# Kernel tuning notes

Measured on AMD Instinct MI355X. Metric: run time of the kernel, lower is better.

Reference implementation:

```python
import jax, jax.numpy as jnp
import numpy as np

T, B, IN_DIM = 8192, 4, 512
D_V, D_K, CHUNK = 512, 64, 128
EPS = 1e-8


def setup_inputs() -> dict:
    key = jax.random.key(0)
    ks = jax.random.split(key, 9)
    s = 0.02
    return {
        "x": jax.random.normal(ks[0], (T, B, IN_DIM), jnp.float32),
        "Wv": jax.random.normal(ks[1], (D_V, IN_DIM), jnp.float32) * s,
        "bv": jnp.zeros((D_V,), jnp.float32),
        "Wk": jax.random.normal(ks[2], (D_K, IN_DIM), jnp.float32) * s,
        "bk": jnp.zeros((D_K,), jnp.float32),
        "Wq": jax.random.normal(ks[3], (D_K, IN_DIM), jnp.float32) * s,
        "bq": jnp.zeros((D_K,), jnp.float32),
        "Wa": jax.random.normal(ks[4], (D_K, IN_DIM), jnp.float32) * s,
        "ba": jnp.zeros((D_K,), jnp.float32),
    }


def reference(x, Wv, bv, Wk, bk, Wq, bq, Wa, ba):
    # Projections: x (T, B, in_dim)
    v = x @ Wv.T + bv                      # (T, B, d)
    k = x @ Wk.T + bk                      # (T, B, n)
    q = x @ Wq.T + bq                      # (T, B, n)
    alpha = jax.nn.sigmoid(x @ Wa.T + ba)  # (T, B, n) decay gates

    Tt, Bb = x.shape[0], x.shape[1]
    C = CHUNK
    nC = Tt // C  # T assumed divisible by chunk size

    def to_chunks(a):
        return a.reshape(nC, C, Bb, a.shape[-1])

    vs, ks_, qs, als = to_chunks(v), to_chunks(k), to_chunks(q), to_chunks(alpha)
    causal = jnp.tril(jnp.ones((C, C), dtype=bool))  # (C, C)

    def body(S, inp):
        v_ch, k_ch, q_ch, a_ch = inp  # each (C, B, .)
        # Cumulative decay product within chunk (clamped as in the original)
        p = jnp.cumprod(jnp.maximum(a_ch, EPS), axis=0)      # (C, B, n)
        q_t = q_ch * p                                        # (C, B, n)
        k_t = k_ch / (p + EPS)                                # (C, B, n)
        # Intra-chunk causal attention scores
        A = jnp.einsum('tbn,sbn->bts', q_t, k_t)              # (B, C, C)
        A = jnp.where(causal[None, :, :], A, jnp.zeros((), A.dtype))
        y = jnp.einsum('bts,sbd->tbd', A, v_ch)               # intra-chunk
        y = y + jnp.einsum('bdn,tbn->tbd', S, q_t)            # cross-chunk carry
        # State update to end of chunk
        p_end = p[-1]                                         # (B, n)
        S_writes = jnp.einsum('tbd,tbn->bdn', v_ch, k_t * p_end[None, :, :])
        S_new = S * p_end[:, None, :] + S_writes              # (B, d, n)
        return S_new, y

    S0 = jnp.zeros((Bb, D_V, D_K), x.dtype)
    _, ys = jax.lax.scan(body, S0, (vs, ks_, qs, als))        # ys: (nC, C, B, d)
    return ys.reshape(Tt, Bb, D_V)
```

## Files before the change

### kernel.cpp

```cpp
#include <hip/hip_runtime.h>
#include <math.h>

#define T_DIM 8192
#define B_DIM 4
#define INDIM 512
#define DV 512
#define DK 64
#define CHUNK 128
#define NCH (T_DIM / CHUNK)
#define ROWS (T_DIM * B_DIM)
#define NPAD 768
#define KCAT 192
#define EPSF 1e-8f

typedef float float4_t __attribute__((ext_vector_type(4)));
typedef short short8_t __attribute__((ext_vector_type(8)));
typedef _Float16 half8_t __attribute__((ext_vector_type(8)));

__device__ inline unsigned short f2bf(float f) {
  unsigned int u = __float_as_uint(f);
  unsigned int r = (u + 0x7fffu + ((u >> 16) & 1u)) >> 16;
  return (unsigned short)r;
}
__device__ inline float bf2f(unsigned short h) {
  return __uint_as_float(((unsigned int)h) << 16);
}
__device__ inline unsigned short f2h(float f) {
  _Float16 h = (_Float16)f;
  unsigned short u;
  __builtin_memcpy(&u, &h, 2);
  return u;
}

__device__ inline void gload16(const void* g, void* l) {
  __builtin_amdgcn_global_load_lds(
      (const __attribute__((address_space(1))) void*)g,
      (__attribute__((address_space(3))) void*)l, 16, 0, 0);
}

__global__ __launch_bounds__(256) void cast_kernel(
    const float* __restrict__ x,
    const float* __restrict__ Wv, const float* __restrict__ Wk,
    const float* __restrict__ Wq, const float* __restrict__ Wa,
    const float* __restrict__ bv, const float* __restrict__ bk,
    const float* __restrict__ bq, const float* __restrict__ ba,
    unsigned short* __restrict__ xh, unsigned short* __restrict__ wh,
    float* __restrict__ bcat)
{
  if (blockIdx.x < 16384) {
    const size_t i4 = ((size_t)blockIdx.x * 256 + threadIdx.x) * 4;
    const float4 v = *(const float4*)&x[i4];
    ushort4 h;
    h.x = f2h(v.x); h.y = f2h(v.y); h.z = f2h(v.z); h.w = f2h(v.w);
    *(ushort4*)&xh[i4] = h;
  } else {
    const int t = (blockIdx.x - 16384) * 256 + threadIdx.x;
    const size_t i4 = (size_t)t * 4;
    const int row = (int)(i4 >> 9);
    const int col = (int)(i4 & 511);
    float4 v = {0.f, 0.f, 0.f, 0.f};
    if (row < 512)      v = *(const float4*)&Wv[(size_t)row * INDIM + col];
    else if (row < 576) v = *(const float4*)&Wk[(size_t)(row - 512) * INDIM + col];
    else if (row < 640) v = *(const float4*)&Wq[(size_t)(row - 576) * INDIM + col];
    else if (row < 704) v = *(const float4*)&Wa[(size_t)(row - 640) * INDIM + col];
    ushort4 h;
    h.x = f2h(v.x); h.y = f2h(v.y); h.z = f2h(v.z); h.w = f2h(v.w);
    *(ushort4*)&wh[i4] = h;
    if (t < NPAD) {
      float b = 0.f;
      if (t < 512)      b = bv[t];
      else if (t < 576) b = bk[t - 512];
      else if (t < 640) b = bq[t - 576];
      else if (t < 704) b = ba[t - 640];
      bcat[t] = b;
    }
  }
}

__global__ __launch_bounds__(256) void proj_mfma_kernel(
    const unsigned short* __restrict__ xh, const unsigned short* __restrict__ wh,
    const float* __restrict__ bcat,
    unsigned short* __restrict__ Bt_h, unsigned short* __restrict__ Bt_l,
    float* __restrict__ k_ws, float* __restrict__ q_ws,
    float* __restrict__ a_ws)
{
  __shared__ __align__(16) _Float16 Ah[3][128 * 32];
  __shared__ __align__(16) _Float16 Bh[3][128 * 32];

  const int d     = blockIdx.x;
  const int grp   = d >> 3;
  const int ytile = (d & 7) * 32 + grp / 6;
  const int xtile = grp % 6;
  const int r0 = ytile * 128;
  const int c0 = xtile * 128;

  const int tid  = threadIdx.x;
  const int wave = tid >> 6, lane = tid & 63;
  const int wm   = (wave & 1) * 64, wn = (wave >> 1) * 64;
  const int fm   = lane & 15;
  const int fk   = (lane >> 4) * 8;
  const int g    = lane >> 4;

  float4_t acc[4][4];
#pragma unroll
  for (int i = 0; i < 4; ++i)
#pragma unroll
    for (int j = 0; j < 4; ++j) acc[i][j] = (float4_t)0.0f;

  const int srow = tid >> 2;
  const int scol = (tid & 3) * 8;

  const unsigned short* pA0 = xh + (size_t)(r0 + srow) * INDIM + scol;
  const unsigned short* pA1 = xh + (size_t)(r0 + 64 + srow) * INDIM + scol;
  const unsigned short* pB0 = wh + (size_t)(c0 + srow) * INDIM + scol;
  const unsigned short* pB1 = wh + (size_t)(c0 + 64 + srow) * INDIM + scol;

  auto stage = [&](int buf, int k0) {
    gload16(pA0 + k0, &Ah[buf][tid * 8]);
    gload16(pA1 + k0, &Ah[buf][(256 + tid) * 8]);
    gload16(pB0 + k0, &Bh[buf][tid * 8]);
    gload16(pB1 + k0, &Bh[buf][(256 + tid) * 8]);
  };

  auto compute = [&](int buf) {
    half8_t a[4], b[4];
#pragma unroll
    for (int i = 0; i < 4; ++i)
      a[i] = *(const half8_t*)&Ah[buf][(wm + i * 16 + fm) * 32 + fk];
#pragma unroll
    for (int j = 0; j < 4; ++j)
      b[j] = *(const half8_t*)&Bh[buf][(wn + j * 16 + fm) * 32 + fk];
    __builtin_amdgcn_s_setprio(1);
#pragma unroll
    for (int i = 0; i < 4; ++i)
#pragma unroll
      for (int j = 0; j < 4; ++j)
        acc[i][j] = __builtin_amdgcn_mfma_f32_16x16x32_f16(a[i], b[j], acc[i][j], 0, 0, 0);
    __builtin_amdgcn_s_setprio(0);
  };

  stage(0, 0);
  stage(1, 32);
  int cur = 0;
  for (int t = 0; t < 14; ++t) {
    stage((cur + 2) % 3, (t + 2) * 32);
    asm volatile("s_waitcnt vmcnt(8)" ::: "memory");
    __builtin_amdgcn_s_barrier();
    compute(cur);
    __builtin_amdgcn_s_barrier();
    cur = (cur + 1) % 3;
  }
  asm volatile("s_waitcnt vmcnt(4)" ::: "memory");
  __builtin_amdgcn_s_barrier();
  compute(cur);
  cur = (cur + 1) % 3;
  asm volatile("s_waitcnt vmcnt(0)" ::: "memory");
  __builtin_amdgcn_s_barrier();
  compute(cur);

  if (xtile < 4) {
    unsigned int* Thl = (unsigned int*)&Ah[0][0];
    const int t0 = r0 >> 2;
    const int cb0 = (t0 >> 7) * 4;
    const int s0 = t0 & 127;
    __syncthreads();
    for (int bb = 0; bb < 4; ++bb) {
#pragma unroll
      for (int j = 0; j < 4; ++j) {
        const int d_loc = wn + j * 16 + fm;
        const float bias = bcat[c0 + d_loc];
#pragma unroll
        for (int i = 0; i < 4; ++i) {
          const int trow = (wm >> 2) + i * 4 + g;
          const float val = acc[i][j][bb] + bias;
          const unsigned short h = f2bf(val);
          const unsigned short l = f2bf(val - bf2f(h));
          Thl[d_loc * 34 + trow] = (unsigned int)h | ((unsigned int)l << 16);
        }
      }
      __syncthreads();
#pragma unroll
      for (int q2 = 0; q2 < 4; ++q2) {
        const int task = q2 * 256 + tid;
        const int dd = task >> 3;
        const int tq = task & 7;
        const unsigned int* p = &Thl[dd * 34 + tq * 4];
        const unsigned int w0 = p[0], w1 = p[1], w2 = p[2], w3 = p[3];
        ushort4 hh, ll;
        hh.x = (unsigned short)w0; ll.x = (unsigned short)(w0 >> 16);
        hh.y = (unsigned short)w1; ll.y = (unsigned short)(w1 >> 16);
        hh.z = (unsigned short)w2; ll.z = (unsigned short)(w2 >> 16);
        hh.w = (unsigned short)w3; ll.w = (unsigned short)(w3 >> 16);
        const size_t oa = ((size_t)(cb0 + bb) * DV + c0 + dd) * CHUNK + s0 + tq * 4;
        *(ushort4*)&Bt_h[oa] = hh;
        *(ushort4*)&Bt_l[oa] = ll;
      }
      __syncthreads();
    }
  } else {
#pragma unroll
    for (int j = 0; j < 4; ++j) {
      const int col = c0 + wn + j * 16 + fm;
      if (col >= 704) continue;
      const float bias = bcat[col];
#pragma unroll
      for (int i = 0; i < 4; ++i) {
#pragma unroll
        for (int r = 0; r < 4; ++r) {
          const int row = r0 + wm + i * 16 + g * 4 + r;
          const float val = acc[i][j][r] + bias;
          if (col < 576) {
            k_ws[(size_t)row * DK + col - 512] = val;
          } else if (col < 640) {
            q_ws[(size_t)row * DK + col - 576] = val;
          } else {
            a_ws[(size_t)row * DK + col - 640] = 1.0f / (1.0f + expf(-val));
          }
        }
      }
    }
  }
}

__global__ __launch_bounds__(512) void prep_kernel(
    const float* __restrict__ a_ws, float* __restrict__ k_ws,
    const float* __restrict__ q_ws,
    unsigned short* __restrict__ Acat_h, unsigned short* __restrict__ Acat_l,
    float* __restrict__ pend)
{
  __shared__ float pal[CHUNK][DK];
  const int c = blockIdx.x, b = blockIdx.y;
  const int cb = c * B_DIM + b;
  const int tid = threadIdx.x;

#pragma unroll
  for (int i = 0; i < 4; ++i) {
    const int f = (i * 512 + tid) * 4;
    const int t = f >> 6, n0 = f & 63;
    const float4 av = *(const float4*)&a_ws[(size_t)(c * CHUNK + t) * 256 + b * 64 + n0];
    *(float4*)&pal[t][n0] = av;
  }
  __syncthreads();

  if (tid < 64) {
    float p = 1.0f;
#pragma unroll 4
    for (int t = 0; t < CHUNK; ++t) {
      p *= fmaxf(pal[t][tid], EPSF);
      pal[t][tid] = p;
    }
    pend[c * 256 + b * 64 + tid] = p;
  }
  __syncthreads();

#pragma unroll
  for (int i = 0; i < 4; ++i) {
    const int f = (i * 512 + tid) * 4;
    const int t = f >> 6, n0 = f & 63;
    const float4 qv = *(const float4*)&q_ws[(size_t)(c * CHUNK + t) * 256 + b * 64 + n0];
    const size_t qa = ((size_t)cb * CHUNK + t) * KCAT + 128 + n0;
    float q0 = qv.x * pal[t][n0 + 0];
    float q1 = qv.y * pal[t][n0 + 1];
    float q2 = qv.z * pal[t][n0 + 2];
    float q3 = qv.w * pal[t][n0 + 3];
    ushort4 h, l;
    h.x = f2bf(q0); l.x = f2bf(q0 - bf2f(h.x));
    h.y = f2bf(q1); l.y = f2bf(q1 - bf2f(h.y));
    h.z = f2bf(q2); l.z = f2bf(q2 - bf2f(h.z));
    h.w = f2bf(q3); l.w = f2bf(q3 - bf2f(h.w));
    *(ushort4*)&Acat_h[qa] = h;
    *(ushort4*)&Acat_l[qa] = l;
  }

#pragma unroll
  for (int i = 0; i < 4; ++i) {
    const int f = (i * 512 + tid) * 4;
    const int t = f >> 6, n0 = f & 63;
    const size_t ka = (size_t)(c * CHUNK + t) * 256 + b * 64 + n0;
    float4 kv = *(const float4*)&k_ws[ka];
    kv.x = kv.x / (pal[t][n0 + 0] + EPSF);
    kv.y = kv.y / (pal[t][n0 + 1] + EPSF);
    kv.z = kv.z / (pal[t][n0 + 2] + EPSF);
    kv.w = kv.w / (pal[t][n0 + 3] + EPSF);
    *(float4*)&k_ws[ka] = kv;
  }
}

__global__ __launch_bounds__(256) void wchunk_mfma_kernel(
    const unsigned short* __restrict__ Bt_h, const unsigned short* __restrict__ Bt_l,
    const float* __restrict__ k_ws, const float* __restrict__ pend,
    float* __restrict__ W_ws)
{
  __shared__ __align__(16) unsigned short Ah[128 * 32];
  __shared__ __align__(16) unsigned short Al[128 * 32];

  const int bd = blockIdx.x;
  const int cb = (bd >> 5) * 8 + (bd & 7);
  const int dt = (bd >> 3) & 3;
  const int c = cb >> 2, b = cb & 3;
  const int tid  = threadIdx.x;
  const int wave = tid >> 6, lane = tid & 63;
  const int wm   = (wave & 1) * 64;
  const int wn   = (wave >> 1) * 32;
  const int fm   = lane & 15;
  const int fk   = (lane >> 4) * 8;

  const unsigned short* Ab_h = Bt_h + ((size_t)cb * DV + dt * 128) * CHUNK;
  const unsigned short* Ab_l = Bt_l + ((size_t)cb * DV + dt * 128) * CHUNK;

  float4_t acc[4][2];
#pragma unroll
  for (int i = 0; i < 4; ++i)
#pragma unroll
    for (int j = 0; j < 2; ++j) acc[i][j] = (float4_t)0.0f;

  for (int ks = 0; ks < 4; ++ks) {
    const int k0 = ks * 32;
#pragma unroll
    for (int q = 0; q < 2; ++q) {
      const int flat = (q * 256 + tid) * 8;
      const int row = flat >> 5, col = flat & 31;
      gload16(&Ab_h[(size_t)row * CHUNK + k0 + col], &Ah[flat]);
      gload16(&Ab_l[(size_t)row * CHUNK + k0 + col], &Al[flat]);
    }

    short8_t b_hi[2], b_lo[2];
#pragma unroll
    for (int j = 0; j < 2; ++j) {
      const int n = wn + j * 16 + fm;
#pragma unroll
      for (int e = 0; e < 8; ++e) {
        const float kv = k_ws[(size_t)(c * CHUNK + k0 + fk + e) * 256 + b * 64 + n];
        const unsigned short h = f2bf(kv);
        b_hi[j][e] = (short)h;
        b_lo[j][e] = (short)f2bf(kv - bf2f(h));
      }
    }
    __syncthreads();

    short8_t a_hi[4], a_lo[4];
#pragma unroll
    for (int i = 0; i < 4; ++i) {
      const int ar = (wm + i * 16 + fm) * 32 + fk;
      a_hi[i] = *(const short8_t*)&Ah[ar];
      a_lo[i] = *(const short8_t*)&Al[ar];
    }
#pragma unroll
    for (int i = 0; i < 4; ++i)
#pragma unroll
      for (int j = 0; j < 2; ++j) {
        acc[i][j] = __builtin_amdgcn_mfma_f32_16x16x32_bf16(a_hi[i], b_hi[j], acc[i][j], 0, 0, 0);
        acc[i][j] = __builtin_amdgcn_mfma_f32_16x16x32_bf16(a_lo[i], b_hi[j], acc[i][j], 0, 0, 0);
        acc[i][j] = __builtin_amdgcn_mfma_f32_16x16x32_bf16(a_hi[i], b_lo[j], acc[i][j], 0, 0, 0);
      }
    __syncthreads();
  }

#pragma unroll
  for (int j = 0; j < 2; ++j) {
    const int n = wn + j * 16 + fm;
    const float pj = pend[c * 256 + b * 64 + n];
#pragma unroll
    for (int i = 0; i < 4; ++i) {
#pragma unroll
      for (int r = 0; r < 4; ++r) {
        const int dd = dt * 128 + wm + i * 16 + (lane >> 4) * 4 + r;
        W_ws[((size_t)cb * DV + dd) * DK + n] = acc[i][j][r] * pj;
      }
    }
  }
}

__global__ __launch_bounds__(256) void scan_kernel(
    const float* __restrict__ W_ws, const float* __restrict__ pend,
    unsigned short* __restrict__ Sh, unsigned short* __restrict__ Sl)
{
  const int flat = blockIdx.x * 256 + threadIdx.x;
  const int n = flat & 63;
  const int bd = flat >> 6;
  const int b = bd >> 9;
  float s = 0.0f;
  for (int c = 0; c < NCH; ++c) {
    const int off = c * 131072 + flat;
    const float w = W_ws[off];
    const unsigned short h = f2bf(s);
    Sh[off] = h;
    Sl[off] = f2bf(s - bf2f(h));
    s = s * pend[c * 256 + b * 64 + n] + w;
  }
}

__global__ __launch_bounds__(256) void score_mfma_kernel(
    const float* __restrict__ k_ws,
    unsigned short* __restrict__ Acat_h, unsigned short* __restrict__ Acat_l)
{
  __shared__ __align__(16) unsigned short Ah[128 * 64];
  __shared__ __align__(16) unsigned short Al[128 * 64];
  __shared__ __align__(16) unsigned short Bh[128 * 64];
  __shared__ __align__(16) unsigned short Bl[128 * 64];

  const int c = blockIdx.x, b = blockIdx.y;
  const int cb = c * B_DIM + b;
  const int tid  = threadIdx.x;
  const int wave = tid >> 6, lane = tid & 63;
  const int wm   = (wave & 1) * 64, wn = (wave >> 1) * 64;
  const int fm   = lane & 15;
  const int fk   = (lane >> 4) * 8;

  const unsigned short* Aq_h = Acat_h + (size_t)cb * CHUNK * KCAT + 128;
  const unsigned short* Aq_l = Acat_l + (size_t)cb * CHUNK * KCAT + 128;

  const int srow = tid >> 3;
  const int scolB = (tid & 7) * 16;
  const int sc = (scolB ^ ((srow & 7) << 4)) >> 1;
  const int sdst = srow * 64 + (scolB >> 1);
#pragma unroll
  for (int q = 0; q < 4; ++q) {
    const int row = q * 32 + srow;
    const int dst = q * 2048 + sdst;
    gload16(&Aq_h[(size_t)row * KCAT + sc], &Ah[dst]);
    gload16(&Aq_l[(size_t)row * KCAT + sc], &Al[dst]);
  }
#pragma unroll
  for (int q = 0; q < 8; ++q) {
    const int f = (q * 256 + tid) * 4;
    const int s = f >> 6, n0 = f & 63;
    const float4 kv = *(const float4*)&k_ws[(size_t)(c * CHUNK + s) * 256 + b * 64 + n0];
    ushort4 h, l;
    h.x = f2bf(kv.x); l.x = f2bf(kv.x - bf2f(h.x));
    h.y = f2bf(kv.y); l.y = f2bf(kv.y - bf2f(h.y));
    h.z = f2bf(kv.z); l.z = f2bf(kv.z - bf2f(h.z));
    h.w = f2bf(kv.w); l.w = f2bf(kv.w - bf2f(h.w));
    const int wi = s * 64 + (n0 ^ ((s & 7) << 3));
    *(ushort4*)&Bh[wi] = h;
    *(ushort4*)&Bl[wi] = l;
  }
  __syncthreads();

  float4_t acc[4][4];
#pragma unroll
  for (int i = 0; i < 4; ++i)
#pragma unroll
    for (int j = 0; j < 4; ++j) acc[i][j] = (float4_t)0.0f;

#pragma unroll
  for (int ksub = 0; ksub < 2; ++ksub) {
    short8_t a_hi[4], a_lo[4], b_hi[4], b_lo[4];
#pragma unroll
    for (int i = 0; i < 4; ++i) {
      const int r = wm + i * 16 + fm;
      const int ar = r * 64 + ((ksub * 32 + fk) ^ ((r & 7) << 3));
      a_hi[i] = *(const short8_t*)&Ah[ar];
      a_lo[i] = *(const short8_t*)&Al[ar];
    }
#pragma unroll
    for (int j = 0; j < 4; ++j) {
      const int r = wn + j * 16 + fm;
      const int br = r * 64 + ((ksub * 32 + fk) ^ ((r & 7) << 3));
      b_hi[j] = *(const short8_t*)&Bh[br];
      b_lo[j] = *(const short8_t*)&Bl[br];
    }
    __builtin_amdgcn_s_setprio(1);
#pragma unroll
    for (int i = 0; i < 4; ++i)
#pragma unroll
      for (int j = 0; j < 4; ++j) {
        acc[i][j] = __builtin_amdgcn_mfma_f32_16x16x32_bf16(a_hi[i], b_hi[j], acc[i][j], 0, 0, 0);
        acc[i][j] = __builtin_amdgcn_mfma_f32_16x16x32_bf16(a_lo[i], b_hi[j], acc[i][j], 0, 0, 0);
        acc[i][j] = __builtin_amdgcn_mfma_f32_16x16x32_bf16(a_hi[i], b_lo[j], acc[i][j], 0, 0, 0);
      }
    __builtin_amdgcn_s_setprio(0);
  }

#pragma unroll
  for (int j = 0; j < 4; ++j) {
    const int s = wn + j * 16 + fm;
#pragma unroll
    for (int i = 0; i < 4; ++i) {
#pragma unroll
      for (int r = 0; r < 4; ++r) {
        const int t = wm + i * 16 + (lane >> 4) * 4 + r;
        const float vv = (s <= t) ? acc[i][j][r] : 0.0f;
        const unsigned short h = f2bf(vv);
        const size_t oa = ((size_t)cb * CHUNK + t) * KCAT + s;
        Acat_h[oa] = h;
        Acat_l[oa] = f2bf(vv - bf2f(h));
      }
    }
  }
}

__global__ __launch_bounds__(256) void out_mfma_kernel(
    const unsigned short* __restrict__ Acat_h, const unsigned short* __restrict__ Acat_l,
    const unsigned short* __restrict__ Bt_h, const unsigned short* __restrict__ Bt_l,
    const unsigned short* __restrict__ Sh, const unsigned short* __restrict__ Sl,
    float* __restrict__ out)
{
  __shared__ __align__(16) unsigned short Ah[128 * 64];
  __shared__ __align__(16) unsigned short Al[128 * 64];
  __shared__ __align__(16) unsigned short Bh[128 * 64];
  __shared__ __align__(16) unsigned short Bl[128 * 64];

  const int bd = blockIdx.x;
  const int cb = (bd >> 5) * 8 + (bd & 7);
  const int nt = (bd >> 3) & 3;
  const int c = cb >> 2, b = cb & 3;
  const int tid  = threadIdx.x;
  const int wave = tid >> 6, lane = tid & 63;
  const int wm   = (wave & 1) * 64, wn = (wave >> 1) * 64;
  const int fm   = lane & 15;
  const int fk   = (lane >> 4) * 8;

  const unsigned short* Ab_h = Acat_h + (size_t)cb * CHUNK * KCAT;
  const unsigned short* Ab_l = Acat_l + (size_t)cb * CHUNK * KCAT;
  const unsigned short* Bb_h = Bt_h + ((size_t)cb * DV + nt * 128) * CHUNK;
  const unsigned short* Bb_l = Bt_l + ((size_t)cb * DV + nt * 128) * CHUNK;
  const unsigned short* Sb_h = Sh + ((size_t)cb * DV + nt * 128) * DK;
  const unsigned short* Sb_l = Sl + ((size_t)cb * DV + nt * 128) * DK;

  const int srow = tid >> 3;
  const int scolB = (tid & 7) * 16;
  const int sc = (scolB ^ ((srow & 7) << 4)) >> 1;
  const int sdst = srow * 64 + (scolB >> 1);

  float4_t acc[4][4];
#pragma unroll
  for (int i = 0; i < 4; ++i)
#pragma unroll
    for (int j = 0; j < 4; ++j) acc[i][j] = (float4_t)0.0f;

  for (int ks = 0; ks < 3; ++ks) {
    const int k0 = ks * 64;
#pragma unroll
    for (int q = 0; q < 4; ++q) {
      const int row = q * 32 + srow;
      const int dst = q * 2048 + sdst;
      gload16(&Ab_h[(size_t)row * KCAT + k0 + sc], &Ah[dst]);
      gload16(&Ab_l[(size_t)row * KCAT + k0 + sc], &Al[dst]);
      if (ks < 2) {
        gload16(&Bb_h[(size_t)row * CHUNK + k0 + sc], &Bh[dst]);
        gload16(&Bb_l[(size_t)row * CHUNK + k0 + sc], &Bl[dst]);
      } else {
        gload16(&Sb_h[(size_t)row * DK + sc], &Bh[dst]);
        gload16(&Sb_l[(size_t)row * DK + sc], &Bl[dst]);
      }
    }
    __syncthreads();

#pragma unroll
    for (int ksub = 0; ksub < 2; ++ksub) {
      short8_t a_hi[4], a_lo[4], b_hi[4], b_lo[4];
#pragma unroll
      for (int i = 0; i < 4; ++i) {
        const int r = wm + i * 16 + fm;
        const int ar = r * 64 + ((ksub * 32 + fk) ^ ((r & 7) << 3));
        a_hi[i] = *(const short8_t*)&Ah[ar];
        a_lo[i] = *(const short8_t*)&Al[ar];
      }
#pragma unroll
      for (int j = 0; j < 4; ++j) {
        const int r = wn + j * 16 + fm;
        const int br = r * 64 + ((ksub * 32 + fk) ^ ((r & 7) << 3));
        b_hi[j] = *(const short8_t*)&Bh[br];
        b_lo[j] = *(const short8_t*)&Bl[br];
      }
      __builtin_amdgcn_s_setprio(1);
#pragma unroll
      for (int i = 0; i < 4; ++i)
#pragma unroll
        for (int j = 0; j < 4; ++j) {
          acc[i][j] = __builtin_amdgcn_mfma_f32_16x16x32_bf16(a_hi[i], b_hi[j], acc[i][j], 0, 0, 0);
          acc[i][j] = __builtin_amdgcn_mfma_f32_16x16x32_bf16(a_lo[i], b_hi[j], acc[i][j], 0, 0, 0);
          acc[i][j] = __builtin_amdgcn_mfma_f32_16x16x32_bf16(a_hi[i], b_lo[j], acc[i][j], 0, 0, 0);
        }
      __builtin_amdgcn_s_setprio(0);
    }
    __syncthreads();
  }

#pragma unroll
  for (int j = 0; j < 4; ++j) {
    const int d = nt * 128 + wn + j * 16 + fm;
#pragma unroll
    for (int i = 0; i < 4; ++i) {
#pragma unroll
      for (int r = 0; r < 4; ++r) {
        const int t = c * CHUNK + wm + i * 16 + (lane >> 4) * 4 + r;
        out[((size_t)t * B_DIM + b) * DV + d] = acc[i][j][r];
      }
    }
  }
}

extern "C" void kernel_launch(void* const* d_in, const int* in_sizes, int n_in,
                              void* d_out, int out_size, void* d_ws, size_t ws_size,
                              hipStream_t stream)
{
  const float* x  = (const float*)d_in[0];
  const float* Wv = (const float*)d_in[1];
  const float* bv = (const float*)d_in[2];
  const float* Wk = (const float*)d_in[3];
  const float* bk = (const float*)d_in[4];
  const float* Wq = (const float*)d_in[5];
  const float* bq = (const float*)d_in[6];
  const float* Wa = (const float*)d_in[7];
  const float* ba = (const float*)d_in[8];
  float* out = (float*)d_out;

  float* ws   = (float*)d_ws;
  unsigned short* Bt_h = (unsigned short*)ws;
  unsigned short* Bt_l = Bt_h + (size_t)NCH * B_DIM * DV * CHUNK;
  float* k_ws = ws + (size_t)ROWS * DV;
  float* a_ws = k_ws + (size_t)ROWS * DK;
  float* pend = a_ws + (size_t)ROWS * DK;
  float* W_ws = pend + NCH * B_DIM * DK;
  float* bcat = W_ws + (size_t)NCH * B_DIM * DV * DK;
  unsigned short* Acat_h = (unsigned short*)(bcat + NPAD);
  unsigned short* Acat_l = Acat_h + (size_t)NCH * B_DIM * CHUNK * KCAT;
  unsigned short* uni = Acat_l + (size_t)NCH * B_DIM * CHUNK * KCAT;
  unsigned short* xh = uni;
  unsigned short* wh = xh + (size_t)ROWS * INDIM;
  float* q_ws = (float*)(uni + (size_t)18 * 1024 * 1024);
  unsigned short* S_h = uni;
  unsigned short* S_l = S_h + (size_t)NCH * B_DIM * DV * DK;

  cast_kernel<<<16384 + 384, 256, 0, stream>>>(
      x, Wv, Wk, Wq, Wa, bv, bk, bq, ba, xh, wh, bcat);
  proj_mfma_kernel<<<(ROWS / 128) * (NPAD / 128), 256, 0, stream>>>(
      xh, wh, bcat, Bt_h, Bt_l, k_ws, q_ws, a_ws);
  prep_kernel<<<dim3(NCH, B_DIM), 512, 0, stream>>>(
      a_ws, k_ws, q_ws, Acat_h, Acat_l, pend);
  wchunk_mfma_kernel<<<NCH * B_DIM * 4, 256, 0, stream>>>(
      Bt_h, Bt_l, k_ws, pend, W_ws);
  scan_kernel<<<(B_DIM * DV * DK) / 256, 256, 0, stream>>>(
      W_ws, pend, S_h, S_l);
  score_mfma_kernel<<<dim3(NCH, B_DIM), 256, 0, stream>>>(
      k_ws, Acat_h, Acat_l);
  out_mfma_kernel<<<NCH * B_DIM * 4, 256, 0, stream>>>(
      Acat_h, Acat_l, Bt_h, Bt_l, S_h, S_l, out);
}
```

Before: 269.9 us.

## Fuse score computation into prep kernel and precompute transposed split-bf16 k

Moves the intra-chunk q·k score MFMA into prep_kernel, which already holds the scaled q and k in shared memory, and drops the separate score kernel launch. Prep also writes k in a transposed hi/lo bf16 layout so wchunk can load it with vector loads into shared memory instead of doing strided scalar fp32 loads and per-element conversion. This cuts a launch, the k_ws round trip and redundant conversions. In exchange prep uses more shared memory (about 96KB) with 512 threads for only 256 blocks, which may lower occupancy.

```diff
diff --git a/kernel.cpp b/kernel.cpp
--- a/kernel.cpp
+++ b/kernel.cpp
@@ -223,15 +223,26 @@
 }
 
 __global__ __launch_bounds__(512) void prep_kernel(
-    const float* __restrict__ a_ws, float* __restrict__ k_ws,
+    const float* __restrict__ a_ws, const float* __restrict__ k_ws,
     const float* __restrict__ q_ws,
     unsigned short* __restrict__ Acat_h, unsigned short* __restrict__ Acat_l,
+    unsigned short* __restrict__ kT_h, unsigned short* __restrict__ kT_l,
     float* __restrict__ pend)
 {
   __shared__ float pal[CHUNK][DK];
+  __shared__ __align__(16) unsigned short Aq_h[128 * 64];
+  __shared__ __align__(16) unsigned short Aq_l[128 * 64];
+  __shared__ __align__(16) unsigned short Bk_h[128 * 64];
+  __shared__ __align__(16) unsigned short Bk_l[128 * 64];
+
   const int c = blockIdx.x, b = blockIdx.y;
   const int cb = c * B_DIM + b;
   const int tid = threadIdx.x;
+  const int wave = tid >> 6, lane = tid & 63;
+  const int wm = (wave & 1) * 64, wn = (wave >> 1) * 32;
+  const int fm = lane & 15;
+  const int fk = (lane >> 4) * 8;
+  const int g  = lane >> 4;
 
 #pragma unroll
   for (int i = 0; i < 4; ++i) {
@@ -270,34 +281,123 @@
     h.w = f2bf(q3); l.w = f2bf(q3 - bf2f(h.w));
     *(ushort4*)&Acat_h[qa] = h;
     *(ushort4*)&Acat_l[qa] = l;
+    const int wi = t * 64 + (n0 ^ ((t & 7) << 3));
+    *(ushort4*)&Aq_h[wi] = h;
+    *(ushort4*)&Aq_l[wi] = l;
   }
 
 #pragma unroll
   for (int i = 0; i < 4; ++i) {
     const int f = (i * 512 + tid) * 4;
     const int t = f >> 6, n0 = f & 63;
-    const size_t ka = (size_t)(c * CHUNK + t) * 256 + b * 64 + n0;
-    float4 kv = *(const float4*)&k_ws[ka];
-    kv.x = kv.x / (pal[t][n0 + 0] + EPSF);
-    kv.y = kv.y / (pal[t][n0 + 1] + EPSF);
-    kv.z = kv.z / (pal[t][n0 + 2] + EPSF);
-    kv.w = kv.w / (pal[t][n0 + 3] + EPSF);
-    *(float4*)&k_ws[ka] = kv;
+    const float4 kv = *(const float4*)&k_ws[(size_t)(c * CHUNK + t) * 256 + b * 64 + n0];
+    float k0 = kv.x / (pal[t][n0 + 0] + EPSF);
+    float k1 = kv.y / (pal[t][n0 + 1] + EPSF);
+    float k2 = kv.z / (pal[t][n0 + 2] + EPSF);
+    float k3 = kv.w / (pal[t][n0 + 3] + EPSF);
+    ushort4 h, l;
+    h.x = f2bf(k0); l.x = f2bf(k0 - bf2f(h.x));
+    h.y = f2bf(k1); l.y = f2bf(k1 - bf2f(h.y));
+    h.z = f2bf(k2); l.z = f2bf(k2 - bf2f(h.z));
+    h.w = f2bf(k3); l.w = f2bf(k3 - bf2f(h.w));
+    const int wi = t * 64 + (n0 ^ ((t & 7) << 3));
+    *(ushort4*)&Bk_h[wi] = h;
+    *(ushort4*)&Bk_l[wi] = l;
+  }
+  __syncthreads();
+
+#pragma unroll
+  for (int it = 0; it < 2; ++it) {
+    const int task = it * 512 + tid;
+    const int n  = task >> 4;
+    const int tg = task & 15;
+    ushort4 h0, h1, l0, l1;
+    unsigned short hh[8], ll[8];
+#pragma unroll
+    for (int e = 0; e < 8; ++e) {
+      const int wi = (tg * 8 + e) * 64 + (n ^ (e << 3));
+      hh[e] = Bk_h[wi];
+      ll[e] = Bk_l[wi];
+    }
+    h0.x = hh[0]; h0.y = hh[1]; h0.z = hh[2]; h0.w = hh[3];
+    h1.x = hh[4]; h1.y = hh[5]; h1.z = hh[6]; h1.w = hh[7];
+    l0.x = ll[0]; l0.y = ll[1]; l0.z = ll[2]; l0.w = ll[3];
+    l1.x = ll[4]; l1.y = ll[5]; l1.z = ll[6]; l1.w = ll[7];
+    const size_t oa = ((size_t)cb * DK + n) * CHUNK + tg * 8;
+    *(ushort4*)&kT_h[oa]     = h0;
+    *(ushort4*)&kT_h[oa + 4] = h1;
+    *(ushort4*)&kT_l[oa]     = l0;
+    *(ushort4*)&kT_l[oa + 4] = l1;
+  }
+
+  float4_t acc[4][2];
+#pragma unroll
+  for (int i = 0; i < 4; ++i)
+#pragma unroll
+    for (int j = 0; j < 2; ++j) acc[i][j] = (float4_t)0.0f;
+
+#pragma unroll
+  for (int ksub = 0; ksub < 2; ++ksub) {
+    short8_t a_hi[4], a_lo[4], b_hi[2], b_lo[2];
+#pragma unroll
+    for (int i = 0; i < 4; ++i) {
+      const int r = wm + i * 16 + fm;
+      const int ar = r * 64 + ((ksub * 32 + fk) ^ ((r & 7) << 3));
+      a_hi[i] = *(const short8_t*)&Aq_h[ar];
+      a_lo[i] = *(const short8_t*)&Aq_l[ar];
+    }
+#pragma unroll
+    for (int j = 0; j < 2; ++j) {
+      const int r = wn + j * 16 + fm;
+      const int br = r * 64 + ((ksub * 32 + fk) ^ ((r & 7) << 3));
+      b_hi[j] = *(const short8_t*)&Bk_h[br];
+      b_lo[j] = *(const short8_t*)&Bk_l[br];
+    }
+    __builtin_amdgcn_s_setprio(1);
+#pragma unroll
+    for (int i = 0; i < 4; ++i)
+#pragma unroll
+      for (int j = 0; j < 2; ++j) {
+        acc[i][j] = __builtin_amdgcn_mfma_f32_16x16x32_bf16(a_hi[i], b_hi[j], acc[i][j], 0, 0, 0);
+        acc[i][j] = __builtin_amdgcn_mfma_f32_16x16x32_bf16(a_lo[i], b_hi[j], acc[i][j], 0, 0, 0);
+        acc[i][j] = __builtin_amdgcn_mfma_f32_16x16x32_bf16(a_hi[i], b_lo[j], acc[i][j], 0, 0, 0);
+      }
+    __builtin_amdgcn_s_setprio(0);
+  }
+
+#pragma unroll
+  for (int j = 0; j < 2; ++j) {
+    const int s = wn + j * 16 + fm;
+#pragma unroll
+    for (int i = 0; i < 4; ++i) {
+#pragma unroll
+      for (int r = 0; r < 4; ++r) {
+        const int t = wm + i * 16 + g * 4 + r;
+        const float vv = (s <= t) ? acc[i][j][r] : 0.0f;
+        const unsigned short h = f2bf(vv);
+        const size_t oa = ((size_t)cb * CHUNK + t) * KCAT + s;
+        Acat_h[oa] = h;
+        Acat_l[oa] = f2bf(vv - bf2f(h));
+      }
+    }
   }
 }
 
 __global__ __launch_bounds__(256) void wchunk_mfma_kernel(
     const unsigned short* __restrict__ Bt_h, const unsigned short* __restrict__ Bt_l,
-    const float* __restrict__ k_ws, const float* __restrict__ pend,
-    float* __restrict__ W_ws)
+    const unsigned short* __restrict__ kT_h, const unsigned short* __restrict__ kT_l,
+    const float* __restrict__ pend, float* __restrict__ W_ws)
 {
   __shared__ __align__(16) unsigned short Ah[128 * 32];
   __shared__ __align__(16) unsigned short Al[128 * 32];
+  __shared__ __align__(16) unsigned short Kh[64 * 128];
+  __shared__ __align__(16) unsigned short Kl[64 * 128];
 
   const int bd = blockIdx.x;
   const int cb = (bd >> 5) * 8 + (bd & 7);
   const int dt = (bd >> 3) & 3;
   const int c = cb >> 2, b = cb & 3;
+  (void)c; (void)b;
   const int tid  = threadIdx.x;
   const int wave = tid >> 6, lane = tid & 63;
   const int wm   = (wave & 1) * 64;
@@ -307,6 +407,16 @@
 
   const unsigned short* Ab_h = Bt_h + ((size_t)cb * DV + dt * 128) * CHUNK;
   const unsigned short* Ab_l = Bt_l + ((size_t)cb * DV + dt * 128) * CHUNK;
+  const unsigned short* Kb_h = kT_h + (size_t)cb * DK * CHUNK;
+  const unsigned short* Kb_l = kT_l + (size_t)cb * DK * CHUNK;
+
+#pragma unroll
+  for (int it = 0; it < 4; ++it) {
+    const int tk = it * 256 + tid;
+    const int n = tk >> 4, slot = tk & 15;
+    gload16(&Kb_h[(size_t)n * CHUNK + ((slot ^ (n & 15)) << 3)], &Kh[tk * 8]);
+    gload16(&Kb_l[(size_t)n * CHUNK + ((slot ^ (n & 15)) << 3)], &Kl[tk * 8]);
+  }
 
   float4_t acc[4][2];
 #pragma unroll
@@ -323,22 +433,9 @@
       gload16(&Ab_h[(size_t)row * CHUNK + k0 + col], &Ah[flat]);
       gload16(&Ab_l[(size_t)row * CHUNK + k0 + col], &Al[flat]);
     }
-
-    short8_t b_hi[2], b_lo[2];
-#pragma unroll
-    for (int j = 0; j < 2; ++j) {
-      const int n = wn + j * 16 + fm;
-#pragma unroll
-      for (int e = 0; e < 8; ++e) {
-        const float kv = k_ws[(size_t)(c * CHUNK + k0 + fk + e) * 256 + b * 64 + n];
-        const unsigned short h = f2bf(kv);
-        b_hi[j][e] = (short)h;
-        b_lo[j][e] = (short)f2bf(kv - bf2f(h));
-      }
-    }
     __syncthreads();
 
-    short8_t a_hi[4], a_lo[4];
+    short8_t a_hi[4], a_lo[4], b_hi[2], b_lo[2];
 #pragma unroll
     for (int i = 0; i < 4; ++i) {
       const int ar = (wm + i * 16 + fm) * 32 + fk;
@@ -346,6 +443,14 @@
       a_lo[i] = *(const short8_t*)&Al[ar];
     }
 #pragma unroll
+    for (int j = 0; j < 2; ++j) {
+      const int n = wn + j * 16 + fm;
+      const int slot = (k0 + fk) >> 3;
+      const int addr = n * CHUNK + ((slot ^ (n & 15)) << 3);
+      b_hi[j] = *(const short8_t*)&Kh[addr];
+      b_lo[j] = *(const short8_t*)&Kl[addr];
+    }
+#pragma unroll
     for (int i = 0; i < 4; ++i)
 #pragma unroll
       for (int j = 0; j < 2; ++j) {
@@ -359,7 +464,7 @@
 #pragma unroll
   for (int j = 0; j < 2; ++j) {
     const int n = wn + j * 16 + fm;
-    const float pj = pend[c * 256 + b * 64 + n];
+    const float pj = pend[(cb >> 2) * 256 + (cb & 3) * 64 + n];
 #pragma unroll
     for (int i = 0; i < 4; ++i) {
 #pragma unroll
@@ -390,106 +495,6 @@
   }
 }
 
-__global__ __launch_bounds__(256) void score_mfma_kernel(
-    const float* __restrict__ k_ws,
-    unsigned short* __restrict__ Acat_h, unsigned short* __restrict__ Acat_l)
-{
-  __shared__ __align__(16) unsigned short Ah[128 * 64];
-  __shared__ __align__(16) unsigned short Al[128 * 64];
-  __shared__ __align__(16) unsigned short Bh[128 * 64];
-  __shared__ __align__(16) unsigned short Bl[128 * 64];
-
-  const int c = blockIdx.x, b = blockIdx.y;
-  const int cb = c * B_DIM + b;
-  const int tid  = threadIdx.x;
-  const int wave = tid >> 6, lane = tid & 63;
-  const int wm   = (wave & 1) * 64, wn = (wave >> 1) * 64;
-  const int fm   = lane & 15;
-  const int fk   = (lane >> 4) * 8;
-
-  const unsigned short* Aq_h = Acat_h + (size_t)cb * CHUNK * KCAT + 128;
-  const unsigned short* Aq_l = Acat_l + (size_t)cb * CHUNK * KCAT + 128;
-
-  const int srow = tid >> 3;
-  const int scolB = (tid & 7) * 16;
-  const int sc = (scolB ^ ((srow & 7) << 4)) >> 1;
-  const int sdst = srow * 64 + (scolB >> 1);
-#pragma unroll
-  for (int q = 0; q < 4; ++q) {
-    const int row = q * 32 + srow;
-    const int dst = q * 2048 + sdst;
-    gload16(&Aq_h[(size_t)row * KCAT + sc], &Ah[dst]);
-    gload16(&Aq_l[(size_t)row * KCAT + sc], &Al[dst]);
-  }
-#pragma unroll
-  for (int q = 0; q < 8; ++q) {
-    const int f = (q * 256 + tid) * 4;
-    const int s = f >> 6, n0 = f & 63;
-    const float4 kv = *(const float4*)&k_ws[(size_t)(c * CHUNK + s) * 256 + b * 64 + n0];
-    ushort4 h, l;
-    h.x = f2bf(kv.x); l.x = f2bf(kv.x - bf2f(h.x));
-    h.y = f2bf(kv.y); l.y = f2bf(kv.y - bf2f(h.y));
-    h.z = f2bf(kv.z); l.z = f2bf(kv.z - bf2f(h.z));
-    h.w = f2bf(kv.w); l.w = f2bf(kv.w - bf2f(h.w));
-    const int wi = s * 64 + (n0 ^ ((s & 7) << 3));
-    *(ushort4*)&Bh[wi] = h;
-    *(ushort4*)&Bl[wi] = l;
-  }
-  __syncthreads();
-
-  float4_t acc[4][4];
-#pragma unroll
-  for (int i = 0; i < 4; ++i)
-#pragma unroll
-    for (int j = 0; j < 4; ++j) acc[i][j] = (float4_t)0.0f;
-
-#pragma unroll
-  for (int ksub = 0; ksub < 2; ++ksub) {
-    short8_t a_hi[4], a_lo[4], b_hi[4], b_lo[4];
-#pragma unroll
-    for (int i = 0; i < 4; ++i) {
-      const int r = wm + i * 16 + fm;
-      const int ar = r * 64 + ((ksub * 32 + fk) ^ ((r & 7) << 3));
-      a_hi[i] = *(const short8_t*)&Ah[ar];
-      a_lo[i] = *(const short8_t*)&Al[ar];
-    }
-#pragma unroll
-    for (int j = 0; j < 4; ++j) {
-      const int r = wn + j * 16 + fm;
-      const int br = r * 64 + ((ksub * 32 + fk) ^ ((r & 7) << 3));
-      b_hi[j] = *(const short8_t*)&Bh[br];
-      b_lo[j] = *(const short8_t*)&Bl[br];
-    }
-    __builtin_amdgcn_s_setprio(1);
-#pragma unroll
-    for (int i = 0; i < 4; ++i)
-#pragma unroll
-      for (int j = 0; j < 4; ++j) {
-        acc[i][j] = __builtin_amdgcn_mfma_f32_16x16x32_bf16(a_hi[i], b_hi[j], acc[i][j], 0, 0, 0);
-        acc[i][j] = __builtin_amdgcn_mfma_f32_16x16x32_bf16(a_lo[i], b_hi[j], acc[i][j], 0, 0, 0);
-        acc[i][j] = __builtin_amdgcn_mfma_f32_16x16x32_bf16(a_hi[i], b_lo[j], acc[i][j], 0, 0, 0);
-      }
-    __builtin_amdgcn_s_setprio(0);
-  }
-
-#pragma unroll
-  for (int j = 0; j < 4; ++j) {
-    const int s = wn + j * 16 + fm;
-#pragma unroll
-    for (int i = 0; i < 4; ++i) {
-#pragma unroll
-      for (int r = 0; r < 4; ++r) {
-        const int t = wm + i * 16 + (lane >> 4) * 4 + r;
-        const float vv = (s <= t) ? acc[i][j][r] : 0.0f;
-        const unsigned short h = f2bf(vv);
-        const size_t oa = ((size_t)cb * CHUNK + t) * KCAT + s;
-        Acat_h[oa] = h;
-        Acat_l[oa] = f2bf(vv - bf2f(h));
-      }
-    }
-  }
-}
-
 __global__ __launch_bounds__(256) void out_mfma_kernel(
     const unsigned short* __restrict__ Acat_h, const unsigned short* __restrict__ Acat_l,
     const unsigned short* __restrict__ Bt_h, const unsigned short* __restrict__ Bt_l,
@@ -621,6 +626,8 @@
   unsigned short* xh = uni;
   unsigned short* wh = xh + (size_t)ROWS * INDIM;
   float* q_ws = (float*)(uni + (size_t)18 * 1024 * 1024);
+  unsigned short* kT_h = (unsigned short*)(q_ws + (size_t)ROWS * DK);
+  unsigned short* kT_l = kT_h + (size_t)NCH * B_DIM * DK * CHUNK;
   unsigned short* S_h = uni;
   unsigned short* S_l = S_h + (size_t)NCH * B_DIM * DV * DK;
 
@@ -629,13 +636,11 @@
   proj_mfma_kernel<<<(ROWS / 128) * (NPAD / 128), 256, 0, stream>>>(
       xh, wh, bcat, Bt_h, Bt_l, k_ws, q_ws, a_ws);
   prep_kernel<<<dim3(NCH, B_DIM), 512, 0, stream>>>(
-      a_ws, k_ws, q_ws, Acat_h, Acat_l, pend);
+      a_ws, k_ws, q_ws, Acat_h, Acat_l, kT_h, kT_l, pend);
   wchunk_mfma_kernel<<<NCH * B_DIM * 4, 256, 0, stream>>>(
-      Bt_h, Bt_l, k_ws, pend, W_ws);
+      Bt_h, Bt_l, kT_h, kT_l, pend, W_ws);
   scan_kernel<<<(B_DIM * DV * DK) / 256, 256, 0, stream>>>(
       W_ws, pend, S_h, S_l);
-  score_mfma_kernel<<<dim3(NCH, B_DIM), 256, 0, stream>>>(
-      k_ws, Acat_h, Acat_l);
   out_mfma_kernel<<<NCH * B_DIM * 4, 256, 0, stream>>>(
       Acat_h, Acat_l, Bt_h, Bt_l, S_h, S_l, out);
 }
```

Result: faster. 260.1 us (-3.6%).
